# Kernel optimization log

Hardware: AMD Instinct MI355X
Metric: run time of the kernel (lower is better)

Reference implementation:

```python
import jax, jax.numpy as jnp
import numpy as np

N, V, T, C_IN, C_OUT, REL, H4, H5 = 256, 25, 128, 64, 64, 9, 18, 6


def setup_inputs() -> dict:
    key = jax.random.key(0)
    ks = jax.random.split(key, 12)

    def w(k, shape, fan_in):
        return (jax.random.normal(k, shape, jnp.float32) / np.sqrt(fan_in)).astype(jnp.float32)

    return {
        "x": jax.random.normal(ks[0], (N, V, T, C_IN), jnp.float32),
        "A": jax.random.uniform(ks[1], (V, V), dtype=jnp.float32),
        "W1": w(ks[2], (C_IN, REL), C_IN), "b1": jnp.zeros((REL,), jnp.float32),
        "W2": w(ks[3], (C_IN, REL), C_IN), "b2": jnp.zeros((REL,), jnp.float32),
        "W3": w(ks[4], (C_IN, REL), C_IN), "b3": jnp.zeros((REL,), jnp.float32),
        "W4a": w(ks[5], (REL, H4), REL), "b4a": jnp.zeros((H4,), jnp.float32),
        "W4b": w(ks[6], (H4, REL), H4), "b4b": jnp.zeros((REL,), jnp.float32),
        "W5a": w(ks[7], (REL, H5), REL), "b5a": jnp.zeros((H5,), jnp.float32),
        "W5b": w(ks[8], (H5, C_OUT), H5), "b5b": jnp.zeros((C_OUT,), jnp.float32),
    }


def reference(x, A, W1, b1, W2, b2, W3, b3, W4a, b4a, W4b, b4b, W5a, b5a, W5b, b5b):
    silu = jax.nn.silu
    alpha = 1.0
    # x: (N, V, T, C) channels-last; Linear projections to rel channels
    x1 = x @ W1 + b1                       # (N, V, T, R)
    x2 = x @ W2 + b2                       # (N, V, T, R)
    x3 = x @ W3 + b3                       # (N, V, T, R)
    # temporal mean (original: transpose(1,3).mean(-2))
    m1 = x1.mean(axis=2)                   # (N, V, R)
    m2 = x2.mean(axis=2)                   # (N, V, R)
    # pairwise joint affinity via broadcast difference
    rel = m1[:, :, None, :] - m2[:, None, :, :]   # (N, V, V, R)
    # small MLP (Linear4) on channel dim
    h = silu(rel @ W4a + b4a)              # (N, V, V, 18)
    h = silu(h @ W4b + b4b)                # (N, V, V, R)
    # scale + static adjacency (broadcast over batch and channels)
    h = h * alpha + A[None, :, :, None]    # (N, V, V, R)
    # einsum 'ncuv,nctv->nctu' in channels-last form: aggregate over v
    agg = jnp.einsum('nuvc,nvtc->nutc', h, x3)    # (N, V, T, R)
    # output MLP (Linear5)
    y = silu(agg @ W5a + b5a)              # (N, V, T, 6)
    y = silu(y @ W5b + b5b)                # (N, V, T, C_out)
    return y
```

## Files before the change

### kernel.cpp

```cpp
#include <hip/hip_runtime.h>
#include <hip/hip_fp16.h>

#define NN 256
#define VV 25
#define TT 128
#define CIN 64
#define CO 64
#define RR 9
#define HH4 18
#define HH5 6
#define TQ 32
#define NT 4

typedef unsigned int uint;

__device__ __forceinline__ float silu_f(float v) {
  return __fdividef(v, 1.0f + __expf(-v));
}
__device__ __forceinline__ __half2 u2h(uint u) {
  union { uint x; __half2 h; } c; c.x = u; return c.h;
}
__device__ __forceinline__ uint h2u(__half2 h) {
  union { __half2 h; uint x; } c; c.h = h; return c.x;
}

__global__ __launch_bounds__(128, 2) void k1_proj(
    const float* __restrict__ x, const float* __restrict__ W3,
    const float* __restrict__ b3, uint* __restrict__ x3g,
    float* __restrict__ xm) {
  const int blk = blockIdx.x;
  const int n = blk / VV, v = blk - n * VV;
  const int tid = threadIdx.x;
  __shared__ __align__(16) float xt[TT * 68];
  __shared__ __align__(16) float xmp[2][64];

  const float4* src = (const float4*)(x + (size_t)blk * TT * CIN);
  float4 r[16];
  #pragma unroll
  for (int k = 0; k < 16; ++k) r[k] = src[k * 128 + tid];
  #pragma unroll
  for (int k = 0; k < 16; ++k) {
    const int idx = k * 128 + tid;
    const int t = idx >> 4, c = (idx & 15) * 4;
    *(float4*)(xt + t * 68 + c) = r[k];
  }
  float4 cs = r[0];
  #pragma unroll
  for (int k = 1; k < 16; ++k) {
    cs.x += r[k].x; cs.y += r[k].y; cs.z += r[k].z; cs.w += r[k].w;
  }
  #pragma unroll
  for (int m = 16; m < 64; m <<= 1) {
    cs.x += __shfl_xor(cs.x, m); cs.y += __shfl_xor(cs.y, m);
    cs.z += __shfl_xor(cs.z, m); cs.w += __shfl_xor(cs.w, m);
  }
  if ((tid & 63) < 16) *(float4*)(&xmp[tid >> 6][(tid & 15) * 4]) = cs;
  __syncthreads();
  if (tid < 64) xm[(size_t)blk * 64 + tid] = xmp[0][tid] + xmp[1][tid];

  float acc[RR];
  #pragma unroll
  for (int j = 0; j < RR; ++j) acc[j] = b3[j];
  const float* xrow = xt + tid * 68;
  #pragma unroll
  for (int c4 = 0; c4 < 16; ++c4) {
    const float4 xv = *(const float4*)(xrow + c4 * 4);
    #pragma unroll
    for (int j = 0; j < RR; ++j) {
      acc[j] = fmaf(xv.x, W3[(c4 * 4 + 0) * RR + j], acc[j]);
      acc[j] = fmaf(xv.y, W3[(c4 * 4 + 1) * RR + j], acc[j]);
      acc[j] = fmaf(xv.z, W3[(c4 * 4 + 2) * RR + j], acc[j]);
      acc[j] = fmaf(xv.w, W3[(c4 * 4 + 3) * RR + j], acc[j]);
    }
  }
  uint w0 = h2u(__floats2half2_rn(acc[0], acc[1]));
  uint w1 = h2u(__floats2half2_rn(acc[2], acc[3]));
  uint w2 = h2u(__floats2half2_rn(acc[4], acc[5]));
  uint w3 = h2u(__floats2half2_rn(acc[6], acc[7]));
  uint w4 = h2u(__floats2half2_rn(acc[8], 0.f));
  uint* dst = x3g +
      ((((size_t)n * NT + (tid >> 5)) * VV + v) * TQ + (tid & 31)) * 6;
  ((uint2*)dst)[0] = make_uint2(w0, w1);
  ((uint2*)dst)[1] = make_uint2(w2, w3);
  ((uint2*)dst)[2] = make_uint2(w4, 0u);
}

__global__ __launch_bounds__(128) void k2_h(
    const float* __restrict__ xm, const float* __restrict__ A,
    const float* __restrict__ W1, const float* __restrict__ b1,
    const float* __restrict__ W2, const float* __restrict__ b2,
    const float* __restrict__ W4a, const float* __restrict__ b4a,
    const float* __restrict__ W4b, const float* __restrict__ b4b,
    uint* __restrict__ h2g) {
  const int n = blockIdx.x;
  const int tid = threadIdx.x;
  __shared__ float m1[VV][RR + 1];
  __shared__ float m2[VV][RR + 1];
  const float* xmn = xm + (size_t)n * VV * CIN;
  for (int i = tid; i < 2 * VV * RR; i += 128) {
    const int which = (i >= VV * RR);
    const int idx = which ? i - VV * RR : i;
    const int v = idx / RR, c = idx - v * RR;
    const float* W = which ? W2 : W1;
    const float* b = which ? b2 : b1;
    const float* row = xmn + v * CIN;
    float s = 0.f;
    #pragma unroll
    for (int k = 0; k < CIN; ++k) s = fmaf(row[k], W[k * RR + c], s);
    s = s * (1.0f / TT) + b[c];
    if (which) m2[v][c] = s; else m1[v][c] = s;
  }
  __syncthreads();
  for (int p = tid; p < VV * VV; p += 128) {
    const int u = p / VV, v2 = p - u * VV;
    float rel[RR];
    #pragma unroll
    for (int j = 0; j < RR; ++j) rel[j] = m1[u][j] - m2[v2][j];
    float t1[HH4];
    #pragma unroll
    for (int k = 0; k < HH4; ++k) {
      float s = b4a[k];
      #pragma unroll
      for (int j = 0; j < RR; ++j) s = fmaf(rel[j], W4a[j * HH4 + k], s);
      t1[k] = silu_f(s);
    }
    const float av = A[u * VV + v2];
    float hc[RR];
    #pragma unroll
    for (int j = 0; j < RR; ++j) {
      float s = b4b[j];
      #pragma unroll
      for (int k = 0; k < HH4; ++k) s = fmaf(t1[k], W4b[k * RR + j], s);
      hc[j] = silu_f(s) + av;
    }
    uint* hp = h2g + ((size_t)n * VV * VV + p) * 6;
    hp[0] = h2u(__floats2half2_rn(hc[0], hc[1]));
    hp[1] = h2u(__floats2half2_rn(hc[2], hc[3]));
    hp[2] = h2u(__floats2half2_rn(hc[4], hc[5]));
    hp[3] = h2u(__floats2half2_rn(hc[6], hc[7]));
    hp[4] = h2u(__floats2half2_rn(hc[8], 0.f));
    hp[5] = 0u;
  }
}

__global__ __launch_bounds__(256, 3) void k3_out(
    const uint* __restrict__ x3g, const uint* __restrict__ h2g,
    const float* __restrict__ W5a, const float* __restrict__ b5a,
    const float* __restrict__ W5b, const float* __restrict__ b5b,
    float* __restrict__ out) {
  const int bid = blockIdx.x;
  const int n = bid >> 2, tq = bid & 3;
  const int tid = threadIdx.x;
  __shared__ __align__(16) uint x3s[VV * TQ * 6];
  __shared__ __align__(16) uint h2s[VV * VV * 6];
  __shared__ __align__(16) uint a5s[VV * TQ * 3];

  const uint* xsrc = x3g + (size_t)bid * (VV * TQ * 6);
  for (int i = tid; i < (VV * TQ * 6) / 4; i += 256)
    ((uint4*)x3s)[i] = ((const uint4*)xsrc)[i];
  const uint* hsrc = h2g + (size_t)n * (VV * VV * 6);
  for (int i = tid; i < VV * VV * 6; i += 256) h2s[i] = hsrc[i];
  __syncthreads();

  for (int p = tid; p < VV * TQ; p += 256) {
    const int u = p >> 5, t = p & 31;
    const uint* xr = x3s + t * 6;
    const uint* hr = h2s + u * VV * 6;
    __half2 c0 = u2h(0u), c1 = c0, c2 = c0, c3 = c0, c4 = c0;
    #pragma unroll 5
    for (int v2 = 0; v2 < VV; ++v2) {
      const uint2 xa = *(const uint2*)(xr + v2 * 192);
      const uint2 xb = *(const uint2*)(xr + v2 * 192 + 2);
      const uint  xc = xr[v2 * 192 + 4];
      const uint2 ha = *(const uint2*)(hr + v2 * 6);
      const uint2 hb = *(const uint2*)(hr + v2 * 6 + 2);
      const uint  hc = hr[v2 * 6 + 4];
      c0 = __hfma2(u2h(ha.x), u2h(xa.x), c0);
      c1 = __hfma2(u2h(ha.y), u2h(xa.y), c1);
      c2 = __hfma2(u2h(hb.x), u2h(xb.x), c2);
      c3 = __hfma2(u2h(hb.y), u2h(xb.y), c3);
      c4 = __hfma2(u2h(hc),   u2h(xc),   c4);
    }
    float ag[RR];
    ag[0] = __low2float(c0); ag[1] = __high2float(c0);
    ag[2] = __low2float(c1); ag[3] = __high2float(c1);
    ag[4] = __low2float(c2); ag[5] = __high2float(c2);
    ag[6] = __low2float(c3); ag[7] = __high2float(c3);
    ag[8] = __low2float(c4);
    float a5v[HH5];
    #pragma unroll
    for (int k = 0; k < HH5; ++k) {
      float s = b5a[k];
      #pragma unroll
      for (int j = 0; j < RR; ++j) s = fmaf(ag[j], W5a[j * HH5 + k], s);
      a5v[k] = silu_f(s);
    }
    a5s[p * 3 + 0] = h2u(__floats2half2_rn(a5v[0], a5v[1]));
    a5s[p * 3 + 1] = h2u(__floats2half2_rn(a5v[2], a5v[3]));
    a5s[p * 3 + 2] = h2u(__floats2half2_rn(a5v[4], a5v[5]));
  }
  __syncthreads();

  const int cq = (tid & 15) * 4;
  float4 wb[HH5];
  #pragma unroll
  for (int k = 0; k < HH5; ++k) wb[k] = *(const float4*)(W5b + k * CO + cq);
  const float4 bb = *(const float4*)(b5b + cq);
  for (int it = 0; it < (VV * TQ) / 16; ++it) {
    const int q = it * 16 + (tid >> 4);
    const int u = q >> 5, t = q & 31;
    const __half2 p01 = u2h(a5s[q * 3 + 0]);
    const __half2 p23 = u2h(a5s[q * 3 + 1]);
    const __half2 p45 = u2h(a5s[q * 3 + 2]);
    const float a0 = __low2float(p01), a1 = __high2float(p01);
    const float a2 = __low2float(p23), a3 = __high2float(p23);
    const float a4 = __low2float(p45), a5 = __high2float(p45);
    float4 y;
    y.x = silu_f(bb.x + a0 * wb[0].x + a1 * wb[1].x + a2 * wb[2].x +
                 a3 * wb[3].x + a4 * wb[4].x + a5 * wb[5].x);
    y.y = silu_f(bb.y + a0 * wb[0].y + a1 * wb[1].y + a2 * wb[2].y +
                 a3 * wb[3].y + a4 * wb[4].y + a5 * wb[5].y);
    y.z = silu_f(bb.z + a0 * wb[0].z + a1 * wb[1].z + a2 * wb[2].z +
                 a3 * wb[3].z + a4 * wb[4].z + a5 * wb[5].z);
    y.w = silu_f(bb.w + a0 * wb[0].w + a1 * wb[1].w + a2 * wb[2].w +
                 a3 * wb[3].w + a4 * wb[4].w + a5 * wb[5].w);
    float* orow = out +
        ((size_t)(n * VV + u) * TT + tq * TQ + t) * CO + cq;
    *(float4*)orow = y;
  }
}

extern "C" void kernel_launch(void* const* d_in, const int* in_sizes, int n_in,
                              void* d_out, int out_size, void* d_ws, size_t ws_size,
                              hipStream_t stream) {
  const float* x   = (const float*)d_in[0];
  const float* A   = (const float*)d_in[1];
  const float* W1  = (const float*)d_in[2];
  const float* b1  = (const float*)d_in[3];
  const float* W2  = (const float*)d_in[4];
  const float* b2  = (const float*)d_in[5];
  const float* W3  = (const float*)d_in[6];
  const float* b3  = (const float*)d_in[7];
  const float* W4a = (const float*)d_in[8];
  const float* b4a = (const float*)d_in[9];
  const float* W4b = (const float*)d_in[10];
  const float* b4b = (const float*)d_in[11];
  const float* W5a = (const float*)d_in[12];
  const float* b5a = (const float*)d_in[13];
  const float* W5b = (const float*)d_in[14];
  const float* b5b = (const float*)d_in[15];
  float* out = (float*)d_out;

  char* ws = (char*)d_ws;
  uint*  x3g = (uint*)ws;
  float* xm  = (float*)(ws + 19660800);
  uint*  h2g = (uint*)(ws + 19660800 + 1638400);

  hipLaunchKernelGGL(k1_proj, dim3(NN * VV), dim3(128), 0, stream,
                     x, W3, b3, x3g, xm);
  hipLaunchKernelGGL(k2_h, dim3(NN), dim3(128), 0, stream,
                     xm, A, W1, b1, W2, b2, W4a, b4a, W4b, b4b, h2g);
  hipLaunchKernelGGL(k3_out, dim3(NN * NT), dim3(256), 0, stream,
                     x3g, h2g, W5a, b5a, W5b, b5b, out);
}
```

Baseline: 162.2 us.

## Fuse affinity MLP kernel into output kernel and repack x3 as planar channels

Drops the separate k2_h launch. Each k3_out block now recomputes the per-batch affinity tensor h (mean projections plus the Linear4 MLP) directly into LDS, so the h2g global round trip goes away. The x3 intermediate switches from an interleaved 6-word-per-element layout to 5 planar channel arrays, which cuts the padding traffic and makes the k1 stores and k3 LDS reads coalesced. In exchange, the h computation is repeated 4 times per batch (once per time-quarter block), and occupancy is raised to 4 blocks per SM through a shared LDS pool.

```diff
diff --git a/kernel.cpp b/kernel.cpp
--- a/kernel.cpp
+++ b/kernel.cpp
@@ -73,113 +73,109 @@
       acc[j] = fmaf(xv.w, W3[(c4 * 4 + 3) * RR + j], acc[j]);
     }
   }
-  uint w0 = h2u(__floats2half2_rn(acc[0], acc[1]));
-  uint w1 = h2u(__floats2half2_rn(acc[2], acc[3]));
-  uint w2 = h2u(__floats2half2_rn(acc[4], acc[5]));
-  uint w3 = h2u(__floats2half2_rn(acc[6], acc[7]));
-  uint w4 = h2u(__floats2half2_rn(acc[8], 0.f));
-  uint* dst = x3g +
-      ((((size_t)n * NT + (tid >> 5)) * VV + v) * TQ + (tid & 31)) * 6;
-  ((uint2*)dst)[0] = make_uint2(w0, w1);
-  ((uint2*)dst)[1] = make_uint2(w2, w3);
-  ((uint2*)dst)[2] = make_uint2(w4, 0u);
-}
-
-__global__ __launch_bounds__(128) void k2_h(
-    const float* __restrict__ xm, const float* __restrict__ A,
+  uint w[5];
+  w[0] = h2u(__floats2half2_rn(acc[0], acc[1]));
+  w[1] = h2u(__floats2half2_rn(acc[2], acc[3]));
+  w[2] = h2u(__floats2half2_rn(acc[4], acc[5]));
+  w[3] = h2u(__floats2half2_rn(acc[6], acc[7]));
+  w[4] = h2u(__floats2half2_rn(acc[8], 0.f));
+  const int tq = tid >> 5, t = tid & 31;
+  uint* dst = x3g + (size_t)(n * NT + tq) * (5 * VV * TQ) + v * TQ + t;
+  #pragma unroll
+  for (int c = 0; c < 5; ++c) dst[c * (VV * TQ)] = w[c];
+}
+
+__global__ __launch_bounds__(256, 4) void k3_out(
+    const uint* __restrict__ x3g, const float* __restrict__ xm,
+    const float* __restrict__ A,
     const float* __restrict__ W1, const float* __restrict__ b1,
     const float* __restrict__ W2, const float* __restrict__ b2,
     const float* __restrict__ W4a, const float* __restrict__ b4a,
     const float* __restrict__ W4b, const float* __restrict__ b4b,
-    uint* __restrict__ h2g) {
-  const int n = blockIdx.x;
-  const int tid = threadIdx.x;
-  __shared__ float m1[VV][RR + 1];
-  __shared__ float m2[VV][RR + 1];
-  const float* xmn = xm + (size_t)n * VV * CIN;
-  for (int i = tid; i < 2 * VV * RR; i += 128) {
-    const int which = (i >= VV * RR);
-    const int idx = which ? i - VV * RR : i;
-    const int v = idx / RR, c = idx - v * RR;
-    const float* W = which ? W2 : W1;
-    const float* b = which ? b2 : b1;
-    const float* row = xmn + v * CIN;
-    float s = 0.f;
-    #pragma unroll
-    for (int k = 0; k < CIN; ++k) s = fmaf(row[k], W[k * RR + c], s);
-    s = s * (1.0f / TT) + b[c];
-    if (which) m2[v][c] = s; else m1[v][c] = s;
-  }
-  __syncthreads();
-  for (int p = tid; p < VV * VV; p += 128) {
-    const int u = p / VV, v2 = p - u * VV;
-    float rel[RR];
-    #pragma unroll
-    for (int j = 0; j < RR; ++j) rel[j] = m1[u][j] - m2[v2][j];
-    float t1[HH4];
-    #pragma unroll
-    for (int k = 0; k < HH4; ++k) {
-      float s = b4a[k];
-      #pragma unroll
-      for (int j = 0; j < RR; ++j) s = fmaf(rel[j], W4a[j * HH4 + k], s);
-      t1[k] = silu_f(s);
-    }
-    const float av = A[u * VV + v2];
-    float hc[RR];
-    #pragma unroll
-    for (int j = 0; j < RR; ++j) {
-      float s = b4b[j];
-      #pragma unroll
-      for (int k = 0; k < HH4; ++k) s = fmaf(t1[k], W4b[k * RR + j], s);
-      hc[j] = silu_f(s) + av;
-    }
-    uint* hp = h2g + ((size_t)n * VV * VV + p) * 6;
-    hp[0] = h2u(__floats2half2_rn(hc[0], hc[1]));
-    hp[1] = h2u(__floats2half2_rn(hc[2], hc[3]));
-    hp[2] = h2u(__floats2half2_rn(hc[4], hc[5]));
-    hp[3] = h2u(__floats2half2_rn(hc[6], hc[7]));
-    hp[4] = h2u(__floats2half2_rn(hc[8], 0.f));
-    hp[5] = 0u;
-  }
-}
-
-__global__ __launch_bounds__(256, 3) void k3_out(
-    const uint* __restrict__ x3g, const uint* __restrict__ h2g,
     const float* __restrict__ W5a, const float* __restrict__ b5a,
     const float* __restrict__ W5b, const float* __restrict__ b5b,
     float* __restrict__ out) {
   const int bid = blockIdx.x;
   const int n = bid >> 2, tq = bid & 3;
   const int tid = threadIdx.x;
-  __shared__ __align__(16) uint x3s[VV * TQ * 6];
-  __shared__ __align__(16) uint h2s[VV * VV * 6];
-  __shared__ __align__(16) uint a5s[VV * TQ * 3];
-
-  const uint* xsrc = x3g + (size_t)bid * (VV * TQ * 6);
-  for (int i = tid; i < (VV * TQ * 6) / 4; i += 256)
-    ((uint4*)x3s)[i] = ((const uint4*)xsrc)[i];
-  const uint* hsrc = h2g + (size_t)n * (VV * VV * 6);
-  for (int i = tid; i < VV * VV * 6; i += 256) h2s[i] = hsrc[i];
+  __shared__ __align__(16) uint pool[9525];
+  uint* x3s = pool;
+  uint* a5s = pool + 4000;
+  float* m12 = (float*)(pool + 4000);
+  float* xmL = (float*)(pool + 4500);
+  uint* h_lds = pool + 6400;
+
+  {
+    const uint4* xsrc = (const uint4*)(x3g + (size_t)bid * 4000);
+    for (int i = tid; i < 1000; i += 256) ((uint4*)x3s)[i] = xsrc[i];
+    const float4* msrc = (const float4*)(xm + (size_t)n * VV * CIN);
+    for (int i = tid; i < 400; i += 256) ((float4*)xmL)[i] = msrc[i];
+  }
+  __syncthreads();
+
+  for (int i = tid; i < 2 * VV * RR; i += 256) {
+    const int which = (i >= VV * RR);
+    const int idx = which ? i - VV * RR : i;
+    const int v = idx / RR, c = idx - v * RR;
+    const float* W = which ? W2 : W1;
+    const float* b = which ? b2 : b1;
+    const float* row = xmL + v * CIN;
+    float s = 0.f;
+    #pragma unroll
+    for (int k = 0; k < CIN; ++k) s = fmaf(row[k], W[k * RR + c], s);
+    m12[(which * VV + v) * 10 + c] = s * (1.0f / TT) + b[c];
+  }
+  __syncthreads();
+
+  for (int p = tid; p < VV * VV; p += 256) {
+    const int u = p / VV, v2 = p - u * VV;
+    float rel[RR];
+    #pragma unroll
+    for (int j = 0; j < RR; ++j) rel[j] = m12[u * 10 + j] - m12[(VV + v2) * 10 + j];
+    float t1[HH4];
+    #pragma unroll
+    for (int k = 0; k < HH4; ++k) {
+      float s = b4a[k];
+      #pragma unroll
+      for (int j = 0; j < RR; ++j) s = fmaf(rel[j], W4a[j * HH4 + k], s);
+      t1[k] = silu_f(s);
+    }
+    const float av = A[u * VV + v2];
+    float hc[RR];
+    #pragma unroll
+    for (int j = 0; j < RR; ++j) {
+      float s = b4b[j];
+      #pragma unroll
+      for (int k = 0; k < HH4; ++k) s = fmaf(t1[k], W4b[k * RR + j], s);
+      hc[j] = silu_f(s) + av;
+    }
+    uint* hp = h_lds + p * 5;
+    hp[0] = h2u(__floats2half2_rn(hc[0], hc[1]));
+    hp[1] = h2u(__floats2half2_rn(hc[2], hc[3]));
+    hp[2] = h2u(__floats2half2_rn(hc[4], hc[5]));
+    hp[3] = h2u(__floats2half2_rn(hc[6], hc[7]));
+    hp[4] = h2u(__floats2half2_rn(hc[8], 0.f));
+  }
   __syncthreads();
 
   for (int p = tid; p < VV * TQ; p += 256) {
     const int u = p >> 5, t = p & 31;
-    const uint* xr = x3s + t * 6;
-    const uint* hr = h2s + u * VV * 6;
+    const uint* hr = h_lds + u * VV * 5;
     __half2 c0 = u2h(0u), c1 = c0, c2 = c0, c3 = c0, c4 = c0;
     #pragma unroll 5
     for (int v2 = 0; v2 < VV; ++v2) {
-      const uint2 xa = *(const uint2*)(xr + v2 * 192);
-      const uint2 xb = *(const uint2*)(xr + v2 * 192 + 2);
-      const uint  xc = xr[v2 * 192 + 4];
-      const uint2 ha = *(const uint2*)(hr + v2 * 6);
-      const uint2 hb = *(const uint2*)(hr + v2 * 6 + 2);
-      const uint  hc = hr[v2 * 6 + 4];
-      c0 = __hfma2(u2h(ha.x), u2h(xa.x), c0);
-      c1 = __hfma2(u2h(ha.y), u2h(xa.y), c1);
-      c2 = __hfma2(u2h(hb.x), u2h(xb.x), c2);
-      c3 = __hfma2(u2h(hb.y), u2h(xb.y), c3);
-      c4 = __hfma2(u2h(hc),   u2h(xc),   c4);
+      const int xo = v2 * TQ + t;
+      const uint x0 = x3s[xo];
+      const uint x1 = x3s[xo + 800];
+      const uint x2 = x3s[xo + 1600];
+      const uint x3 = x3s[xo + 2400];
+      const uint x4 = x3s[xo + 3200];
+      const uint* hv = hr + v2 * 5;
+      c0 = __hfma2(u2h(hv[0]), u2h(x0), c0);
+      c1 = __hfma2(u2h(hv[1]), u2h(x1), c1);
+      c2 = __hfma2(u2h(hv[2]), u2h(x2), c2);
+      c3 = __hfma2(u2h(hv[3]), u2h(x3), c3);
+      c4 = __hfma2(u2h(hv[4]), u2h(x4), c4);
     }
     float ag[RR];
     ag[0] = __low2float(c0); ag[1] = __high2float(c0);
@@ -253,13 +249,11 @@
 
   char* ws = (char*)d_ws;
   uint*  x3g = (uint*)ws;
-  float* xm  = (float*)(ws + 19660800);
-  uint*  h2g = (uint*)(ws + 19660800 + 1638400);
+  float* xm  = (float*)(ws + 16384000);
 
   hipLaunchKernelGGL(k1_proj, dim3(NN * VV), dim3(128), 0, stream,
                      x, W3, b3, x3g, xm);
-  hipLaunchKernelGGL(k2_h, dim3(NN), dim3(128), 0, stream,
-                     xm, A, W1, b1, W2, b2, W4a, b4a, W4b, b4b, h2g);
   hipLaunchKernelGGL(k3_out, dim3(NN * NT), dim3(256), 0, stream,
-                     x3g, h2g, W5a, b5a, W5b, b5b, out);
-}
+                     x3g, xm, A, W1, b1, W2, b2, W4a, b4a, W4b, b4b,
+                     W5a, b5a, W5b, b5b, out);
+}
```

New measurement: 174.4 us. 7.5% more time.
